# Kernel optimization log

Measured on AMD Instinct MI355X. Metric: run time of the kernel, lower is better.

## Reference

```python
import jax, jax.numpy as jnp
import numpy as np
from jax import lax


def setup_inputs() -> dict:
    key = jax.random.key(0)
    ks = jax.random.split(key, 10)
    B, T, Din, U = 64, 256, 128, 1024
    def rn(k, shape, sc=0.02):
        return jax.random.normal(k, shape, jnp.float32) * sc
    return {
        "inputs": jax.random.normal(ks[0], (B, T, Din), jnp.float32),
        "We1": rn(ks[1], (Din, U)), "be1": jnp.zeros((U,), jnp.float32),
        "We2": rn(ks[2], (U, U)),   "be2": jnp.zeros((U,), jnp.float32),
        "W1": rn(ks[3], (U, U)),    "b1": jnp.zeros((U,), jnp.float32),
        "W2": rn(ks[4], (U, U)),    "b2": jnp.zeros((U,), jnp.float32),
        "V": rn(ks[5], (U, 1)),     "bV": jnp.zeros((1,), jnp.float32),
        "Wk": rn(ks[6], (U, 4 * U)),
        "Wr": rn(ks[7], (U, 4 * U)),
        "bl": jnp.zeros((4 * U,), jnp.float32),
        "Wo": rn(ks[8], (U, 1)),    "bo": jnp.zeros((1,), jnp.float32),
        "seq_len": 256,
    }


def reference(inputs, We1, be1, We2, be2, W1, b1, W2, b2, V, bV,
              Wk, Wr, bl, Wo, bo, seq_len):
    B = inputs.shape[0]
    U = Wr.shape[0]
    f32 = inputs.dtype
    # Frozen embedding ANN, applied per timestep: [B,T,Din] -> [B,T,U]
    h1 = jax.nn.relu(inputs @ We1 + be1)
    x = jax.nn.relu(h1 @ We2 + be2)            # attention values [B,T,U]
    # W2(values) is constant across decode steps; hoist out of the loop.
    keys = x @ W2 + b2                          # [B,T,U]

    def step(carry, _):
        h, c = carry                            # [B,U] each
        # Bahdanau attention: score = V(tanh(W1(q) + W2(values)))
        q = h @ W1 + b1                         # [B,U]
        score = jnp.tanh(q[:, None, :] + keys) @ V + bV   # [B,T,1]
        attw = jax.nn.softmax(score, axis=1)    # softmax over time axis
        ctx = jnp.sum(attw * x, axis=1)         # context vector [B,U]
        # Keras LSTM cell (gate order i,f,g,o; sigmoid recurrent, tanh act)
        z = ctx @ Wk + h @ Wr + bl              # [B,4U]
        i, f, g, o = jnp.split(z, 4, axis=-1)
        i = jax.nn.sigmoid(i)
        f = jax.nn.sigmoid(f)
        g = jnp.tanh(g)
        o = jax.nn.sigmoid(o)
        c_new = f * c + i * g
        h_new = o * jnp.tanh(c_new)
        out = h_new @ Wo + bo                   # [B,1]
        return (h_new, c_new), out

    init = (jnp.zeros((B, U), f32), jnp.zeros((B, U), f32))
    _, outs = lax.scan(step, init, None, length=seq_len)   # [seq_len,B,1]
    return jnp.squeeze(outs, axis=2)            # [seq_len, B]
```

## Files before the change

kernel.cpp:

```cpp
#include <hip/hip_runtime.h>

#define U_ 1024
#define B_ 64
#define T_ 256
#define DIN_ 128
#define BT_ (B_*T_)
#define G_ 1024
#define NWB 576

typedef __attribute__((ext_vector_type(4))) float f32x4;
typedef __attribute__((ext_vector_type(8))) short s16x8;
typedef __attribute__((ext_vector_type(4))) unsigned short u16x4;
typedef unsigned long long u64;

union U64F2 { u64 q; float f[2]; };
union U64H4 { u64 q; unsigned short h[4]; };

__device__ inline unsigned short f2bf(float x){
  unsigned u = __float_as_uint(x);
  u += 0x7FFFu + ((u >> 16) & 1u);
  return (unsigned short)(u >> 16);
}
__device__ inline float bf2f(unsigned short b){ return __uint_as_float(((unsigned)b) << 16); }
__device__ inline float fast_rcp(float x){ return __builtin_amdgcn_rcpf(x); }
__device__ inline float fast_tanh(float x){
  float e = __expf(2.0f * x);
  return 1.0f - 2.0f * fast_rcp(e + 1.0f);
}
__device__ inline float fast_sig(float x){
  return fast_rcp(1.0f + __expf(-x));
}

__device__ inline u64 ald64(const u64* p){
  return __hip_atomic_load((u64*)p, __ATOMIC_RELAXED, __HIP_MEMORY_SCOPE_AGENT);
}
__device__ inline void ast64(u64* p, u64 v){
  __hip_atomic_store(p, v, __ATOMIC_RELAXED, __HIP_MEMORY_SCOPE_AGENT);
}
__device__ inline float aldf(const float* p){
  return __hip_atomic_load((float*)p, __ATOMIC_RELAXED, __HIP_MEMORY_SCOPE_AGENT);
}
__device__ inline void astf(float* p, float v){
  __hip_atomic_store(p, v, __ATOMIC_RELAXED, __HIP_MEMORY_SCOPE_AGENT);
}
__device__ inline s16x8 frag_ald(const u64* p){
  u64 a = ald64(p), b = ald64(p + 1);
  union { u64 q[2]; s16x8 v; } x; x.q[0] = a; x.q[1] = b; return x.v;
}

__device__ inline float score8(s16x8 k0, s16x8 k1, const float* tqv, const float* Vv){
  float s = 0.f;
  #pragma unroll
  for (int e = 0; e < 8; ++e){
    float kf = bf2f((unsigned short)k0[e]);
    float num = tqv[e] + kf;
    float den = fmaf(tqv[e], kf, 1.0f);
    s += Vv[e] * num * fast_rcp(den);
  }
  #pragma unroll
  for (int e = 0; e < 8; ++e){
    float kf = bf2f((unsigned short)k1[e]);
    float num = tqv[8+e] + kf;
    float den = fmaf(tqv[8+e], kf, 1.0f);
    s += Vv[8+e] * num * fast_rcp(den);
  }
  return s;
}

__global__ void init_kernel(float* c, unsigned short* hb0, unsigned short* hb1,
                            unsigned* cnt, unsigned* rel, const float* V, float* vbound){
  int i = blockIdx.x * 256 + threadIdx.x;
  if (i < B_*U_){ c[i] = 0.f; hb0[i] = 0; hb1[i] = 0; }
  if (i < 64*16){ cnt[i] = 0u; rel[i] = 0u; }
  if (blockIdx.x == 0){
    __shared__ float red[4];
    int t = threadIdx.x, lane = t & 63, w = t >> 6;
    float s = fabsf(V[t]) + fabsf(V[t+256]) + fabsf(V[t+512]) + fabsf(V[t+768]);
    #pragma unroll
    for (int mk = 32; mk >= 1; mk >>= 1) s += __shfl_xor(s, mk, 64);
    if (lane == 0) red[w] = s;
    __syncthreads();
    if (t == 0) vbound[0] = red[0] + red[1] + red[2] + red[3];
  }
}

__global__ void transpose_bf_kernel(const float* W, unsigned short* WT, int K, int N){
  int ktiles = K >> 5;
  int kb = blockIdx.x % ktiles, nb = blockIdx.x / ktiles;
  __shared__ float tile[32][33];
  int x = threadIdx.x & 31, y8 = threadIdx.x >> 5;
  #pragma unroll
  for (int i = 0; i < 4; ++i){
    int y = y8*4 + i;
    tile[y][x] = W[(size_t)(kb*32 + y)*N + nb*32 + x];
  }
  __syncthreads();
  #pragma unroll
  for (int i = 0; i < 4; ++i){
    int y = y8*4 + i;
    WT[(size_t)(nb*32 + y)*K + kb*32 + x] = f2bf(tile[x][y]);
  }
}

template<int AF32>
__global__ __launch_bounds__(256) void gemm_embed(const void* Aptr, const unsigned short* BT,
                                                  const float* bias, unsigned short* Cout,
                                                  int K, int act){
  int nb = blockIdx.x & 15, mb = blockIdx.x >> 4;
  int lane = threadIdx.x & 63, w = threadIdx.x >> 6;
  int l15 = lane & 15, quad = lane >> 4;
  int m0 = mb*64 + w*16;
  int arow = m0 + l15;
  f32x4 acc[4];
  #pragma unroll
  for (int nt = 0; nt < 4; ++nt) acc[nt] = (f32x4){0.f,0.f,0.f,0.f};

  for (int k0 = 0; k0 < K; k0 += 32){
    int koff = k0 + quad*8;
    s16x8 a8;
    if (AF32){
      const float* ap = (const float*)Aptr + (size_t)arow*K + koff;
      f32x4 lo = *(const f32x4*)ap;
      f32x4 hi = *(const f32x4*)(ap + 4);
      a8[0]=(short)f2bf(lo[0]); a8[1]=(short)f2bf(lo[1]); a8[2]=(short)f2bf(lo[2]); a8[3]=(short)f2bf(lo[3]);
      a8[4]=(short)f2bf(hi[0]); a8[5]=(short)f2bf(hi[1]); a8[6]=(short)f2bf(hi[2]); a8[7]=(short)f2bf(hi[3]);
    } else {
      a8 = *(const s16x8*)((const unsigned short*)Aptr + (size_t)arow*K + koff);
    }
    #pragma unroll
    for (int nt = 0; nt < 4; ++nt){
      const unsigned short* bp = BT + (size_t)(nb*64 + nt*16 + l15)*K + koff;
      s16x8 b8 = *(const s16x8*)bp;
      acc[nt] = __builtin_amdgcn_mfma_f32_16x16x32_bf16(a8, b8, acc[nt], 0, 0, 0);
    }
  }
  #pragma unroll
  for (int nt = 0; nt < 4; ++nt){
    int col = nb*64 + nt*16 + l15;
    float bv = bias[col];
    #pragma unroll
    for (int r = 0; r < 4; ++r){
      int row = m0 + quad*4 + r;
      float v = acc[nt][r] + bv;
      v = (act == 0) ? fmaxf(v, 0.f) : fast_tanh(v);
      Cout[(size_t)row*U_ + col] = f2bf(v);
    }
  }
}

struct SeqP {
  const unsigned short *W1Tb, *WkTb, *WrTb, *tk, *xv;
  const float *b1, *bl, *V, *Wo, *bo, *vbound;
  float *tq, *ew, *c, *zh, *out_part, *out;
  unsigned short *ctxb, *hb0, *hb1;
  unsigned *cnt, *rel;
};

__device__ inline void gridbar(unsigned* cnt, unsigned* rel, unsigned barno){
  __syncthreads();
  if (threadIdx.x == 0)
    __hip_atomic_fetch_add(&cnt[(blockIdx.x & 63) * 16], 1u, __ATOMIC_RELAXED, __HIP_MEMORY_SCOPE_AGENT);
  if (blockIdx.x == 0){
    if (threadIdx.x < 64){
      const unsigned tgt = barno * G_;
      for (;;){
        unsigned v = __hip_atomic_load(&cnt[threadIdx.x * 16], __ATOMIC_RELAXED, __HIP_MEMORY_SCOPE_AGENT);
        #pragma unroll
        for (int mk = 32; mk >= 1; mk >>= 1) v += __shfl_xor(v, mk, 64);
        if (v >= tgt) break;
        __builtin_amdgcn_s_sleep(2);
      }
      __hip_atomic_store(&rel[threadIdx.x * 16], barno, __ATOMIC_RELAXED, __HIP_MEMORY_SCOPE_AGENT);
    }
  } else if (threadIdx.x == 0){
    unsigned* myrel = &rel[(blockIdx.x & 63) * 16];
    while (__hip_atomic_load(myrel, __ATOMIC_RELAXED, __HIP_MEMORY_SCOPE_AGENT) < barno)
      __builtin_amdgcn_s_sleep(4);
  }
  __syncthreads();
}

__device__ inline void out_reduce(const SeqP& p, int b, int sidx, float* smem,
                                  int t, int lane, int w){
  float v = aldf(&p.out_part[b*256 + t]);
  #pragma unroll
  for (int mk = 32; mk >= 1; mk >>= 1) v += __shfl_xor(v, mk, 64);
  if (lane == 0) smem[w] = v;
  __syncthreads();
  if (t == 0) p.out[sidx*64 + b] = smem[0] + smem[1] + smem[2] + smem[3] + p.bo[0];
  __syncthreads();
}

__global__ __launch_bounds__(256, 4) void seq_kernel(SeqP p){
  const int bi = blockIdx.x;
  const int t  = threadIdx.x;
  const int lane = t & 63, w = t >> 6;
  const int l15 = lane & 15, quad = lane >> 4;
  __shared__ __align__(16) unsigned short lfrag[16384];
  __shared__ __align__(16) float smem[1664];
  unsigned barno = 0;
  const float Mb = p.vbound[0];

  if (bi < NWB){
    const unsigned short* wsrc;
    if (bi < 64)       wsrc = p.W1Tb + (size_t)(bi*16 + l15)*U_;
    else if (bi < 320) wsrc = p.WrTb + (size_t)((bi - 64)*16 + l15)*U_;
    else               wsrc = p.WkTb + (size_t)((l15 >> 2)*U_ + (bi - 320)*4 + (l15 & 3))*U_;
    for (int it = w; it < 32; it += 4)
      *(s16x8*)&lfrag[it*512 + lane*8] = *(const s16x8*)(wsrc + it*32 + quad*8);
  } else {
    const unsigned short* ksrc = p.tk + (size_t)((bi >> 4)*T_ + (bi & 15)*16)*U_;
    for (int r = w; r < 16; r += 4){
      *(s16x8*)&lfrag[r*1024 +       lane*8] = *(const s16x8*)(ksrc + (size_t)r*U_ + lane*16);
      *(s16x8*)&lfrag[r*1024 + 512 + lane*8] = *(const s16x8*)(ksrc + (size_t)r*U_ + lane*16 + 8);
    }
  }
  __syncthreads();

  u64* tqu  = (u64*)p.tq;
  u64* ewu  = (u64*)p.ew;
  u64* zhu  = (u64*)p.zh;
  u64* ctxu = (u64*)p.ctxb;

  for (int step = 0; step < T_; ++step){
    const u64* hbRu = (const u64*)((step & 1) ? p.hb1 : p.hb0);
    u64*       hbWu = (u64*)((step & 1) ? p.hb0 : p.hb1);

    gridbar(p.cnt, p.rel, ++barno);

    if (bi < 64){
      int jcol = bi*16 + l15;
      int rbase = (w*16 + l15) << 8;
      f32x4 acc = (f32x4){0.f,0.f,0.f,0.f};
      #pragma unroll 8
      for (int k = 0; k < U_; k += 32){
        s16x8 a8 = frag_ald(hbRu + rbase + ((k + quad*8) >> 2));
        s16x8 b8 = *(const s16x8*)&lfrag[(k >> 5)*512 + lane*8];
        acc = __builtin_amdgcn_mfma_f32_16x16x32_bf16(a8, b8, acc, 0, 0, 0);
      }
      float bj = p.b1[jcol];
      float* tqs = smem;
      #pragma unroll
      for (int r = 0; r < 4; ++r)
        tqs[l15*68 + w*16 + quad*4 + r] = fast_tanh(acc[r] + bj);
      __syncthreads();
      if (t < 64){
        int ub64 = (t*U_ + bi*16) >> 1;
        #pragma unroll
        for (int cc = 0; cc < 16; cc += 2){
          U64F2 x;
          x.f[0] = tqs[(cc+0)*68 + t];
          x.f[1] = tqs[(cc+1)*68 + t];
          ast64(tqu + ub64 + (cc >> 1), x.q);
        }
      }
    } else if (bi < 320){
      int bz = bi - 64;
      int rbase = (w*16 + l15) << 8;
      int jc0 = bz*16 + l15;
      f32x4 acc0 = (f32x4){0.f,0.f,0.f,0.f};
      #pragma unroll 8
      for (int k = 0; k < U_; k += 32){
        s16x8 a8 = frag_ald(hbRu + rbase + ((k + quad*8) >> 2));
        s16x8 b8 = *(const s16x8*)&lfrag[(k >> 5)*512 + lane*8];
        acc0 = __builtin_amdgcn_mfma_f32_16x16x32_bf16(a8, b8, acc0, 0, 0, 0);
      }
      float bl0 = p.bl[jc0];
      int brow = w*16 + quad*4;
      U64F2 x;
      int i0 = (jc0*64 + brow) >> 1;
      x.f[0] = acc0[0] + bl0; x.f[1] = acc0[1] + bl0; ast64(zhu + i0, x.q);
      x.f[0] = acc0[2] + bl0; x.f[1] = acc0[3] + bl0; ast64(zhu + i0 + 1, x.q);
    } else if (bi >= 960){
      if (step > 0) out_reduce(p, bi - 960, step - 1, smem, t, lane, w);
    }

    gridbar(p.cnt, p.rel, ++barno);

    {
      int b = bi >> 4, tg = bi & 15;
      float tqv[16], Vv[16];
      int tqb = (b*U_ + lane*16) >> 1;
      #pragma unroll
      for (int i = 0; i < 8; ++i){
        U64F2 x; x.q = ald64(tqu + tqb + i);
        tqv[2*i] = x.f[0]; tqv[2*i+1] = x.f[1];
      }
      const float* Vp = p.V + lane*16;
      #pragma unroll
      for (int i = 0; i < 16; i += 4) *(f32x4*)&Vv[i] = *(const f32x4*)(Vp + i);
      int trow = tg*16 + w*4;
      float sr[4];
      if (bi >= NWB){
        #pragma unroll
        for (int rr = 0; rr < 4; ++rr){
          int rl = w*4 + rr;
          s16x8 k0 = *(const s16x8*)&lfrag[rl*1024 +       lane*8];
          s16x8 k1 = *(const s16x8*)&lfrag[rl*1024 + 512 + lane*8];
          sr[rr] = score8(k0, k1, tqv, Vv);
        }
      } else {
        const unsigned short* kp = p.tk + (size_t)(b*T_ + trow)*U_ + lane*16;
        #pragma unroll
        for (int rr = 0; rr < 4; ++rr){
          s16x8 k0 = *(const s16x8*)(kp + (size_t)rr*U_);
          s16x8 k1 = *(const s16x8*)(kp + (size_t)rr*U_ + 8);
          sr[rr] = score8(k0, k1, tqv, Vv);
        }
      }
      #pragma unroll
      for (int mk = 32; mk >= 1; mk >>= 1){
        #pragma unroll
        for (int rr = 0; rr < 4; ++rr) sr[rr] += __shfl_xor(sr[rr], mk, 64);
      }
      if (lane == 0){
        int eb = (b*T_ + trow) >> 1;
        #pragma unroll
        for (int j = 0; j < 2; ++j){
          U64F2 x;
          x.f[0] = __expf(sr[2*j]   - Mb);
          x.f[1] = __expf(sr[2*j+1] - Mb);
          ast64(ewu + eb + j, x.q);
        }
      }
    }

    gridbar(p.cnt, p.rel, ++barno);

    {
      int b = bi >> 4, ug = bi & 15;
      float* ewL = smem;
      float* tmp = smem + 256;
      float* red = smem + 272;
      if (t < 128){
        U64F2 x; x.q = ald64(ewu + b*128 + t);
        ewL[2*t] = x.f[0]; ewL[2*t+1] = x.f[1];
      }
      __syncthreads();
      float e = ewL[t];
      float sum = e;
      #pragma unroll
      for (int mk = 32; mk >= 1; mk >>= 1) sum += __shfl_xor(sum, mk, 64);
      if (lane == 0) tmp[w] = sum;
      __syncthreads();
      float rd = fast_rcp(tmp[0] + tmp[1] + tmp[2] + tmp[3]);

      int ui = t & 15, tgp = t >> 4;
      int u = ug*64 + ui*4;
      const unsigned short* xp = p.xv + (size_t)b*T_*U_ + u;
      f32x4 a = (f32x4){0.f,0.f,0.f,0.f};
      #pragma unroll 4
      for (int t8 = tgp; t8 < T_; t8 += 16){
        float wg = ewL[t8];
        u16x4 x4 = *(const u16x4*)(xp + (size_t)t8*U_);
        a[0] = fmaf(wg, bf2f(x4[0]), a[0]);
        a[1] = fmaf(wg, bf2f(x4[1]), a[1]);
        a[2] = fmaf(wg, bf2f(x4[2]), a[2]);
        a[3] = fmaf(wg, bf2f(x4[3]), a[3]);
      }
      *(f32x4*)&red[(tgp*16 + ui)*4] = a;
      __syncthreads();
      if (t < 16){
        f32x4 r = (f32x4){0.f,0.f,0.f,0.f};
        #pragma unroll
        for (int g = 0; g < 16; ++g){
          f32x4 rr = *(f32x4*)&red[(g*16 + t)*4];
          r[0]+=rr[0]; r[1]+=rr[1]; r[2]+=rr[2]; r[3]+=rr[3];
        }
        U64H4 cv;
        cv.h[0]=f2bf(r[0]*rd); cv.h[1]=f2bf(r[1]*rd); cv.h[2]=f2bf(r[2]*rd); cv.h[3]=f2bf(r[3]*rd);
        ast64(ctxu + b*256 + ug*16 + t, cv.q);
      }
    }

    gridbar(p.cnt, p.rel, ++barno);

    if (bi >= 320 && bi < NWB){
      int cb = bi - 320;
      int ub = cb*4;
      int gate = l15 >> 2, uo = l15 & 3;
      int jcol = gate*U_ + ub + uo;
      int rbase = (w*16 + l15) << 8;
      f32x4 acc = (f32x4){0.f,0.f,0.f,0.f};
      #pragma unroll 8
      for (int k = 0; k < U_; k += 32){
        s16x8 a8 = frag_ald(ctxu + rbase + ((k + quad*8) >> 2));
        s16x8 b8 = *(const s16x8*)&lfrag[(k >> 5)*512 + lane*8];
        acc = __builtin_amdgcn_mfma_f32_16x16x32_bf16(a8, b8, acc, 0, 0, 0);
      }
      int brow = w*16 + quad*4;
      int zi0 = (jcol*64 + brow) >> 1;
      U64F2 z0, z1;
      z0.q = ald64(zhu + zi0); z1.q = ald64(zhu + zi0 + 1);
      acc[0] += z0.f[0]; acc[1] += z0.f[1]; acc[2] += z1.f[0]; acc[3] += z1.f[1];
      float* zs = smem;
      float* hs = smem + 1088;
      float* op = smem + 1344;
      *(f32x4*)&zs[l15*68 + brow] = acc;
      __syncthreads();
      {
        int b = t & 63, ui = t >> 6;
        int u = ub + ui;
        float zi = zs[(0*4 + ui)*68 + b];
        float zf = zs[(1*4 + ui)*68 + b];
        float zg = zs[(2*4 + ui)*68 + b];
        float zo = zs[(3*4 + ui)*68 + b];
        float ig = fast_sig(zi), fg = fast_sig(zf);
        float gg = fast_tanh(zg), og = fast_sig(zo);
        float cold = p.c[u*64 + b];
        float cn = fg*cold + ig*gg;
        float hn = og * fast_tanh(cn);
        p.c[u*64 + b] = cn;
        hs[ui*64 + b] = hn;
        op[ui*64 + b] = hn * p.Wo[u];
      }
      __syncthreads();
      if (t < 64){
        U64H4 h0;
        #pragma unroll
        for (int k = 0; k < 4; ++k) h0.h[k] = f2bf(hs[k*64 + t]);
        ast64(hbWu + t*256 + cb, h0.q);
        float po = op[t] + op[64 + t] + op[128 + t] + op[192 + t];
        astf(&p.out_part[t*256 + cb], po);
      }
    }
  }

  gridbar(p.cnt, p.rel, ++barno);
  if (bi >= 960) out_reduce(p, bi - 960, T_ - 1, smem, t, lane, w);
}

extern "C" void kernel_launch(void* const* d_in, const int* in_sizes, int n_in,
                              void* d_out, int out_size, void* d_ws, size_t ws_size,
                              hipStream_t stream){
  const float* inputs = (const float*)d_in[0];
  const float* We1 = (const float*)d_in[1];
  const float* be1 = (const float*)d_in[2];
  const float* We2 = (const float*)d_in[3];
  const float* be2 = (const float*)d_in[4];
  const float* W1  = (const float*)d_in[5];
  const float* b1  = (const float*)d_in[6];
  const float* W2  = (const float*)d_in[7];
  const float* b2  = (const float*)d_in[8];
  const float* V   = (const float*)d_in[9];
  const float* Wk  = (const float*)d_in[11];
  const float* Wr  = (const float*)d_in[12];
  const float* bl  = (const float*)d_in[13];
  const float* Wo  = (const float*)d_in[14];
  const float* bo  = (const float*)d_in[15];
  float* out = (float*)d_out;

  char* ws = (char*)d_ws;
  size_t off = 0;
  auto alloc = [&](size_t bytes) -> void* {
    void* pp = ws + off;
    off = (off + bytes + 255) & ~(size_t)255;
    return pp;
  };
  unsigned short* We1Tb = (unsigned short*)alloc((size_t)1024*128*2);
  unsigned short* We2Tb = (unsigned short*)alloc((size_t)1024*1024*2);
  unsigned short* W2Tb  = (unsigned short*)alloc((size_t)1024*1024*2);
  unsigned short* W1Tb  = (unsigned short*)alloc((size_t)1024*1024*2);
  unsigned short* WkTb  = (unsigned short*)alloc((size_t)4096*1024*2);
  unsigned short* WrTb  = (unsigned short*)alloc((size_t)4096*1024*2);
  unsigned short* h1tk  = (unsigned short*)alloc((size_t)BT_*U_*2);
  unsigned short* xv    = (unsigned short*)alloc((size_t)BT_*U_*2);
  float*          c     = (float*)alloc((size_t)B_*U_*4);
  unsigned short* hb0   = (unsigned short*)alloc((size_t)B_*U_*2);
  unsigned short* hb1   = (unsigned short*)alloc((size_t)B_*U_*2);
  unsigned short* ctxb  = (unsigned short*)alloc((size_t)B_*U_*2);
  float*          tq    = (float*)alloc((size_t)B_*U_*4);
  float*          ew    = (float*)alloc((size_t)B_*T_*4);
  float*          zh    = (float*)alloc((size_t)4*U_*64*4);
  float*          out_part = (float*)alloc((size_t)64*256*4);
  unsigned*       cnt   = (unsigned*)alloc(64*16*4);
  unsigned*       rel   = (unsigned*)alloc(64*16*4);
  float*          vbound= (float*)alloc(256);
  if (ws_size < off) return;

  init_kernel<<<256, 256, 0, stream>>>(c, hb0, hb1, cnt, rel, V, vbound);
  transpose_bf_kernel<<<(128/32)*(1024/32),  256, 0, stream>>>(We1, We1Tb, 128, 1024);
  transpose_bf_kernel<<<(1024/32)*(1024/32), 256, 0, stream>>>(We2, We2Tb, 1024, 1024);
  transpose_bf_kernel<<<(1024/32)*(1024/32), 256, 0, stream>>>(W2,  W2Tb,  1024, 1024);
  transpose_bf_kernel<<<(1024/32)*(1024/32), 256, 0, stream>>>(W1,  W1Tb,  1024, 1024);
  transpose_bf_kernel<<<(1024/32)*(4096/32), 256, 0, stream>>>(Wk,  WkTb,  1024, 4096);
  transpose_bf_kernel<<<(1024/32)*(4096/32), 256, 0, stream>>>(Wr,  WrTb,  1024, 4096);

  gemm_embed<1><<<4096, 256, 0, stream>>>((const void*)inputs, We1Tb, be1, h1tk, DIN_, 0);
  gemm_embed<0><<<4096, 256, 0, stream>>>((const void*)h1tk,   We2Tb, be2, xv,   U_,   0);
  gemm_embed<0><<<4096, 256, 0, stream>>>((const void*)xv,     W2Tb,  b2,  h1tk, U_,   1);

  SeqP sp;
  sp.W1Tb = W1Tb; sp.WkTb = WkTb; sp.WrTb = WrTb; sp.tk = h1tk; sp.xv = xv;
  sp.b1 = b1; sp.bl = bl; sp.V = V; sp.Wo = Wo; sp.bo = bo; sp.vbound = vbound;
  sp.tq = tq; sp.ew = ew; sp.c = c; sp.zh = zh;
  sp.out_part = out_part; sp.out = out;
  sp.ctxb = ctxb; sp.hb0 = hb0; sp.hb1 = hb1; sp.cnt = cnt; sp.rel = rel;
  seq_kernel<<<dim3(G_), dim3(256), 0, stream>>>(sp);
}
```

Baseline: 12.22 ms.

## Replace grid-wide barriers with fine-grained per-stage dependency flags

The persistent sequence kernel used to run four full grid barriers per decode step. These are replaced with targeted producer/consumer counters and release flags. Blocks now wait only on the stages they depend on: query projection done, per-batch score done, context and z-hidden done, LSTM cell done. Independent work such as the Wr·h GEMM can overlap the attention phases, and barrier latency drops. The cost is more complex ordering logic that relies on relaxed atomics with no explicit fences, so memory visibility between stages is a correctness risk.

```diff
diff --git a/kernel.cpp b/kernel.cpp
--- a/kernel.cpp
+++ b/kernel.cpp
@@ -8,6 +8,16 @@
 #define G_ 1024
 #define NWB 576
 
+#define FA_L   0
+#define RELA_L 64
+#define CE_L   128
+#define CZ_L   192
+#define CX_L   208
+#define RELX_L 272
+#define CC_L   336
+#define RELC_L 352
+#define SYNC_N (416*16)
+
 typedef __attribute__((ext_vector_type(4))) float f32x4;
 typedef __attribute__((ext_vector_type(8))) short s16x8;
 typedef __attribute__((ext_vector_type(4))) unsigned short u16x4;
@@ -43,9 +53,25 @@
 __device__ inline void astf(float* p, float v){
   __hip_atomic_store(p, v, __ATOMIC_RELAXED, __HIP_MEMORY_SCOPE_AGENT);
 }
+__device__ inline unsigned ald32(const unsigned* p){
+  return __hip_atomic_load((unsigned*)p, __ATOMIC_RELAXED, __HIP_MEMORY_SCOPE_AGENT);
+}
+__device__ inline void ast32(unsigned* p, unsigned v){
+  __hip_atomic_store(p, v, __ATOMIC_RELAXED, __HIP_MEMORY_SCOPE_AGENT);
+}
+__device__ inline void aadd32(unsigned* p, unsigned v){
+  __hip_atomic_fetch_add(p, v, __ATOMIC_RELAXED, __HIP_MEMORY_SCOPE_AGENT);
+}
 __device__ inline s16x8 frag_ald(const u64* p){
   u64 a = ald64(p), b = ald64(p + 1);
   union { u64 q[2]; s16x8 v; } x; x.q[0] = a; x.q[1] = b; return x.v;
+}
+
+__device__ inline void wait1(unsigned* line, unsigned tgt){
+  if (threadIdx.x == 0){
+    while (ald32(line) < tgt) __builtin_amdgcn_s_sleep(2);
+  }
+  __syncthreads();
 }
 
 __device__ inline float score8(s16x8 k0, s16x8 k1, const float* tqv, const float* Vv){
@@ -68,10 +94,10 @@
 }
 
 __global__ void init_kernel(float* c, unsigned short* hb0, unsigned short* hb1,
-                            unsigned* cnt, unsigned* rel, const float* V, float* vbound){
+                            unsigned* sync, const float* V, float* vbound){
   int i = blockIdx.x * 256 + threadIdx.x;
   if (i < B_*U_){ c[i] = 0.f; hb0[i] = 0; hb1[i] = 0; }
-  if (i < 64*16){ cnt[i] = 0u; rel[i] = 0u; }
+  if (i < SYNC_N) sync[i] = 0u;
   if (blockIdx.x == 0){
     __shared__ float red[4];
     int t = threadIdx.x, lane = t & 63, w = t >> 6;
@@ -153,32 +179,8 @@
   const float *b1, *bl, *V, *Wo, *bo, *vbound;
   float *tq, *ew, *c, *zh, *out_part, *out;
   unsigned short *ctxb, *hb0, *hb1;
-  unsigned *cnt, *rel;
+  unsigned *sync;
 };
-
-__device__ inline void gridbar(unsigned* cnt, unsigned* rel, unsigned barno){
-  __syncthreads();
-  if (threadIdx.x == 0)
-    __hip_atomic_fetch_add(&cnt[(blockIdx.x & 63) * 16], 1u, __ATOMIC_RELAXED, __HIP_MEMORY_SCOPE_AGENT);
-  if (blockIdx.x == 0){
-    if (threadIdx.x < 64){
-      const unsigned tgt = barno * G_;
-      for (;;){
-        unsigned v = __hip_atomic_load(&cnt[threadIdx.x * 16], __ATOMIC_RELAXED, __HIP_MEMORY_SCOPE_AGENT);
-        #pragma unroll
-        for (int mk = 32; mk >= 1; mk >>= 1) v += __shfl_xor(v, mk, 64);
-        if (v >= tgt) break;
-        __builtin_amdgcn_s_sleep(2);
-      }
-      __hip_atomic_store(&rel[threadIdx.x * 16], barno, __ATOMIC_RELAXED, __HIP_MEMORY_SCOPE_AGENT);
-    }
-  } else if (threadIdx.x == 0){
-    unsigned* myrel = &rel[(blockIdx.x & 63) * 16];
-    while (__hip_atomic_load(myrel, __ATOMIC_RELAXED, __HIP_MEMORY_SCOPE_AGENT) < barno)
-      __builtin_amdgcn_s_sleep(4);
-  }
-  __syncthreads();
-}
 
 __device__ inline void out_reduce(const SeqP& p, int b, int sidx, float* smem,
                                   int t, int lane, int w){
@@ -198,7 +200,7 @@
   const int l15 = lane & 15, quad = lane >> 4;
   __shared__ __align__(16) unsigned short lfrag[16384];
   __shared__ __align__(16) float smem[1664];
-  unsigned barno = 0;
+  unsigned* sync = p.sync;
   const float Mb = p.vbound[0];
 
   if (bi < NWB){
@@ -226,9 +228,8 @@
     const u64* hbRu = (const u64*)((step & 1) ? p.hb1 : p.hb0);
     u64*       hbWu = (u64*)((step & 1) ? p.hb0 : p.hb1);
 
-    gridbar(p.cnt, p.rel, ++barno);
-
     if (bi < 64){
+      wait1(&sync[(RELC_L + (bi & 63))*16], (unsigned)step);
       int jcol = bi*16 + l15;
       int rbase = (w*16 + l15) << 8;
       f32x4 acc = (f32x4){0.f,0.f,0.f,0.f};
@@ -254,7 +255,21 @@
           ast64(tqu + ub64 + (cc >> 1), x.q);
         }
       }
+      __syncthreads();
+      if (t == 0) ast32(&sync[(FA_L + bi)*16], (unsigned)(step + 1));
+      if (bi == 0){
+        if (t < 64){
+          unsigned tgt = (unsigned)(step + 1);
+          for (;;){
+            bool ok = ald32(&sync[(FA_L + t)*16]) >= tgt;
+            if (__ballot(ok) == ~0ull) break;
+            __builtin_amdgcn_s_sleep(1);
+          }
+          ast32(&sync[(RELA_L + t)*16], tgt);
+        }
+      }
     } else if (bi < 320){
+      wait1(&sync[(RELC_L + (bi & 63))*16], (unsigned)step);
       int bz = bi - 64;
       int rbase = (w*16 + l15) << 8;
       int jc0 = bz*16 + l15;
@@ -271,12 +286,30 @@
       int i0 = (jc0*64 + brow) >> 1;
       x.f[0] = acc0[0] + bl0; x.f[1] = acc0[1] + bl0; ast64(zhu + i0, x.q);
       x.f[0] = acc0[2] + bl0; x.f[1] = acc0[3] + bl0; ast64(zhu + i0 + 1, x.q);
+      __syncthreads();
+      if (t == 0) aadd32(&sync[(CZ_L + ((bi - 64) & 15))*16], 1u);
     } else if (bi >= 960){
-      if (step > 0) out_reduce(p, bi - 960, step - 1, smem, t, lane, w);
-    }
-
-    gridbar(p.cnt, p.rel, ++barno);
-
+      if (bi == 960){
+        if (step > 0){
+          if (t < 64){
+            unsigned tgt = 16u * (unsigned)step;
+            for (;;){
+              bool ok = (t < 16) ? (ald32(&sync[(CC_L + t)*16]) >= tgt) : true;
+              if (__ballot(ok) == ~0ull) break;
+              __builtin_amdgcn_s_sleep(1);
+            }
+            ast32(&sync[(RELC_L + t)*16], (unsigned)step);
+          }
+          __syncthreads();
+          out_reduce(p, 0, step - 1, smem, t, lane, w);
+        }
+      } else {
+        wait1(&sync[(RELC_L + (bi & 63))*16], (unsigned)step);
+        if (step > 0) out_reduce(p, bi - 960, step - 1, smem, t, lane, w);
+      }
+    }
+
+    wait1(&sync[(RELA_L + (bi & 63))*16], (unsigned)(step + 1));
     {
       int b = bi >> 4, tg = bi & 15;
       float tqv[16], Vv[16];
@@ -324,9 +357,10 @@
         }
       }
     }
-
-    gridbar(p.cnt, p.rel, ++barno);
-
+    __syncthreads();
+    if (t == 0) aadd32(&sync[(CE_L + (bi >> 4))*16], 1u);
+
+    wait1(&sync[(CE_L + (bi >> 4))*16], 16u * (unsigned)(step + 1));
     {
       int b = bi >> 4, ug = bi & 15;
       float* ewL = smem;
@@ -372,10 +406,30 @@
         ast64(ctxu + b*256 + ug*16 + t, cv.q);
       }
     }
-
-    gridbar(p.cnt, p.rel, ++barno);
+    __syncthreads();
+    if (t == 0) aadd32(&sync[(CX_L + (bi & 63))*16], 1u);
+
+    if (bi == 576){
+      unsigned tgt = 16u * (unsigned)(step + 1);
+      if (w == 0){
+        for (;;){
+          bool ok = ald32(&sync[(CX_L + lane)*16]) >= tgt;
+          if (__ballot(ok) == ~0ull) break;
+          __builtin_amdgcn_s_sleep(1);
+        }
+      } else if (w == 1){
+        for (;;){
+          bool ok = (lane < 16) ? (ald32(&sync[(CZ_L + lane)*16]) >= tgt) : true;
+          if (__ballot(ok) == ~0ull) break;
+          __builtin_amdgcn_s_sleep(1);
+        }
+      }
+      __syncthreads();
+      if (t < 64) ast32(&sync[(RELX_L + t)*16], (unsigned)(step + 1));
+    }
 
     if (bi >= 320 && bi < NWB){
+      wait1(&sync[(RELX_L + (bi & 63))*16], (unsigned)(step + 1));
       int cb = bi - 320;
       int ub = cb*4;
       int gate = l15 >> 2, uo = l15 & 3;
@@ -423,11 +477,27 @@
         float po = op[t] + op[64 + t] + op[128 + t] + op[192 + t];
         astf(&p.out_part[t*256 + cb], po);
       }
-    }
-  }
-
-  gridbar(p.cnt, p.rel, ++barno);
-  if (bi >= 960) out_reduce(p, bi - 960, T_ - 1, smem, t, lane, w);
+      __syncthreads();
+      if (t == 0) aadd32(&sync[(CC_L + ((bi - 320) & 15))*16], 1u);
+    }
+  }
+
+  if (bi == 960){
+    if (t < 64){
+      unsigned tgt = 16u * (unsigned)T_;
+      for (;;){
+        bool ok = (t < 16) ? (ald32(&sync[(CC_L + t)*16]) >= tgt) : true;
+        if (__ballot(ok) == ~0ull) break;
+        __builtin_amdgcn_s_sleep(1);
+      }
+      ast32(&sync[(RELC_L + t)*16], (unsigned)T_);
+    }
+    __syncthreads();
+    out_reduce(p, 0, T_ - 1, smem, t, lane, w);
+  } else if (bi > 960){
+    wait1(&sync[(RELC_L + (bi & 63))*16], (unsigned)T_);
+    out_reduce(p, bi - 960, T_ - 1, smem, t, lane, w);
+  }
 }
 
 extern "C" void kernel_launch(void* const* d_in, const int* in_sizes, int n_in,
@@ -473,12 +543,11 @@
   float*          ew    = (float*)alloc((size_t)B_*T_*4);
   float*          zh    = (float*)alloc((size_t)4*U_*64*4);
   float*          out_part = (float*)alloc((size_t)64*256*4);
-  unsigned*       cnt   = (unsigned*)alloc(64*16*4);
-  unsigned*       rel   = (unsigned*)alloc(64*16*4);
+  unsigned*       sync  = (unsigned*)alloc((size_t)SYNC_N*4);
   float*          vbound= (float*)alloc(256);
   if (ws_size < off) return;
 
-  init_kernel<<<256, 256, 0, stream>>>(c, hb0, hb1, cnt, rel, V, vbound);
+  init_kernel<<<256, 256, 0, stream>>>(c, hb0, hb1, sync, V, vbound);
   transpose_bf_kernel<<<(128/32)*(1024/32),  256, 0, stream>>>(We1, We1Tb, 128, 1024);
   transpose_bf_kernel<<<(1024/32)*(1024/32), 256, 0, stream>>>(We2, We2Tb, 1024, 1024);
   transpose_bf_kernel<<<(1024/32)*(1024/32), 256, 0, stream>>>(W2,  W2Tb,  1024, 1024);
@@ -495,6 +564,6 @@
   sp.b1 = b1; sp.bl = bl; sp.V = V; sp.Wo = Wo; sp.bo = bo; sp.vbound = vbound;
   sp.tq = tq; sp.ew = ew; sp.c = c; sp.zh = zh;
   sp.out_part = out_part; sp.out = out;
-  sp.ctxb = ctxb; sp.hb0 = hb0; sp.hb1 = hb1; sp.cnt = cnt; sp.rel = rel;
+  sp.ctxb = ctxb; sp.hb0 = hb0; sp.hb1 = hb1; sp.sync = sync;
   seq_kernel<<<dim3(G_), dim3(256), 0, stream>>>(sp);
 }
```

Result: slower. 12.61 ms (+3.2%).
